# Performance work log

Hardware: AMD Instinct MI355X
Metric: run time of the kernel (lower is better)

## Reference

```python
import jax, jax.numpy as jnp
import numpy as np

VOCAB, EDIM, WFEAT, LABELS, SLOPE = 50000, 128, 128, 2, 0.01
N = 8192

def setup_inputs() -> dict:
    key = jax.random.key(0)
    ks = jax.random.split(key, 8)
    inSen = jax.random.randint(ks[0], (N,), 0, VOCAB, dtype=jnp.int64) if jax.config.read('jax_enable_x64') else jax.random.randint(ks[0], (N,), 0, VOCAB, dtype=jnp.int32)
    adj = jax.random.randint(ks[1], (N, N), 0, 2, dtype=jnp.int32)
    emb = jax.random.normal(ks[2], (VOCAB, EDIM), dtype=jnp.float32)
    W = jax.random.normal(ks[3], (EDIM, WFEAT), dtype=jnp.float32) * (1.0 / np.sqrt(EDIM))
    a_src = jax.random.normal(ks[4], (WFEAT,), dtype=jnp.float32) * (1.0 / np.sqrt(WFEAT))
    a_dst = jax.random.normal(ks[5], (WFEAT,), dtype=jnp.float32) * (1.0 / np.sqrt(WFEAT))
    cls_W = jax.random.normal(ks[6], (WFEAT, LABELS), dtype=jnp.float32) * (1.0 / np.sqrt(WFEAT))
    cls_b = jax.random.normal(ks[7], (LABELS,), dtype=jnp.float32) * 0.01
    return {"inSen": inSen, "adj": adj, "selfLink": 1, "emb": emb, "W": W,
            "a_src": a_src, "a_dst": a_dst, "cls_W": cls_W, "cls_b": cls_b}

def reference(inSen, adj, selfLink, emb, W, a_src, a_dst, cls_W, cls_b):
    # Embedding lookup: (N, edim)
    words = emb[inSen]
    # GAT layer: linear projection then adjacency-masked additive attention
    h = words @ W                              # (N, wFeat)
    f_src = h @ a_src                          # (N,)
    f_dst = h @ a_dst                          # (N,)
    e = jax.nn.leaky_relu(f_src[:, None] + f_dst[None, :], negative_slope=SLOPE)  # (N, N)
    mask = (adj + selfLink * jnp.eye(adj.shape[0], dtype=adj.dtype)) > 0
    e = jnp.where(mask, e, jnp.float32(-1e9))
    attention = jax.nn.softmax(e, axis=1)      # (N, N)
    sentence = attention @ h                   # (N, wFeat)
    # Max pool over words, classify
    poolSentence = jnp.max(sentence, axis=0)   # (wFeat,)
    label = jax.nn.softmax(poolSentence @ cls_W + cls_b, axis=0)  # (labels,)
    return (poolSentence, attention, sentence, label)
```

## Files before the change

kernel.cpp:

```cpp
#include <hip/hip_runtime.h>
#include <hip/hip_bf16.h>

#define NR 8192
#define WF 128

typedef short bf16x8 __attribute__((ext_vector_type(8)));
typedef float f32x4 __attribute__((ext_vector_type(4)));

static __device__ __forceinline__ unsigned int f2bf(float f) {
    unsigned int u = __float_as_uint(f);
    return (u + 0x7fffu + ((u >> 16) & 1u)) >> 16;
}
static __device__ __forceinline__ void atomicMaxF(float* addr, float v) {
    if (v >= 0.f) atomicMax((int*)addr, __float_as_int(v));
    else          atomicMin((unsigned int*)addr, __float_as_uint(v));
}
static __device__ __forceinline__ float lrelu(float x) { return x > 0.f ? x : 0.01f * x; }

__global__ __launch_bounds__(256) void k_proj(
    const int* __restrict__ inSen, const float* __restrict__ emb,
    const float* __restrict__ W, const float* __restrict__ a_src,
    const float* __restrict__ a_dst, float* __restrict__ f_src,
    float* __restrict__ f_dst, float* __restrict__ maxfd,
    unsigned short* __restrict__ hB)
{
    __shared__ float ht[16 * 132];
    const int t = threadIdx.x;
    const int f = t & 127, rh = t >> 7;
    const int i0 = blockIdx.x * 16;

    int wd[8];
    #pragma unroll
    for (int r = 0; r < 8; ++r) wd[r] = inSen[i0 + rh * 8 + r];
    float h[8];
    #pragma unroll
    for (int r = 0; r < 8; ++r) h[r] = 0.f;

    for (int k4 = 0; k4 < 32; ++k4) {
        const float w0 = W[(k4 * 4 + 0) * WF + f];
        const float w1 = W[(k4 * 4 + 1) * WF + f];
        const float w2 = W[(k4 * 4 + 2) * WF + f];
        const float w3 = W[(k4 * 4 + 3) * WF + f];
        #pragma unroll
        for (int r = 0; r < 8; ++r) {
            float4 ev = ((const float4*)(emb + (size_t)wd[r] * 128))[k4];
            h[r] += ev.x * w0 + ev.y * w1 + ev.z * w2 + ev.w * w3;
        }
    }
    #pragma unroll
    for (int r = 0; r < 8; ++r) ht[(rh * 8 + r) * 132 + f] = h[r];
    __syncthreads();

    if (t < 16) {
        float s = 0.f, d = 0.f;
        for (int k4 = 0; k4 < 32; ++k4) {
            float4 hv = *(const float4*)(ht + t * 132 + k4 * 4);
            float4 as = ((const float4*)a_src)[k4];
            float4 ad = ((const float4*)a_dst)[k4];
            s += hv.x * as.x + hv.y * as.y + hv.z * as.z + hv.w * as.w;
            d += hv.x * ad.x + hv.y * ad.y + hv.z * ad.z + hv.w * ad.w;
        }
        f_src[i0 + t] = s;
        f_dst[i0 + t] = d;
        float dm = d;
        #pragma unroll
        for (int o = 1; o < 16; o <<= 1) dm = fmaxf(dm, __shfl_xor(dm, o));
        if (t == 0) atomicMaxF(maxfd, dm);
    }
    {
        const int kb = blockIdx.x >> 1, half = blockIdx.x & 1;
        const int nf = t >> 5, l32 = t & 31;
        const int qloc = l32 >> 4, fx = l32 & 15;
        const int lane = (half * 2 + qloc) * 16 + fx;
        const float* hp = ht + (qloc * 8) * 132 + nf * 16 + fx;
        uint4 v;
        v.x = f2bf(hp[0 * 132]) | (f2bf(hp[1 * 132]) << 16);
        v.y = f2bf(hp[2 * 132]) | (f2bf(hp[3 * 132]) << 16);
        v.z = f2bf(hp[4 * 132]) | (f2bf(hp[5 * 132]) << 16);
        v.w = f2bf(hp[6 * 132]) | (f2bf(hp[7 * 132]) << 16);
        *(uint4*)(hB + ((size_t)kb * 8 + nf) * 512 + lane * 8) = v;
    }
}

static __device__ __forceinline__ void adj_chunk(
    int c, int4 a, float4 f, int lane, int row, int sl,
    float fs, float C, int shl,
    unsigned int* __restrict__ mrow, float& sum)
{
    const bool m0 = a.x > 0, m1 = a.y > 0, m2 = a.z > 0, m3 = a.w > 0;
    float p0 = m0 ? __expf(lrelu(fs + f.x) - C) : 0.f;
    float p1 = m1 ? __expf(lrelu(fs + f.y) - C) : 0.f;
    float p2 = m2 ? __expf(lrelu(fs + f.z) - C) : 0.f;
    float p3 = m3 ? __expf(lrelu(fs + f.w) - C) : 0.f;
    unsigned int nib = (m0 ? 1u : 0u) | (m1 ? 2u : 0u) | (m2 ? 4u : 0u) | (m3 ? 8u : 0u);
    float ssum = p0 + p1 + p2 + p3;
    if (c == (row >> 8)) {
        if (lane == ((row & 255) >> 2)) {
            const int jd = row & 3;
            const int aj = jd == 0 ? a.x : jd == 1 ? a.y : jd == 2 ? a.z : a.w;
            const float fj = jd == 0 ? f.x : jd == 1 ? f.y : jd == 2 ? f.z : f.w;
            const bool mo = aj > 0, mn = (aj + sl) > 0;
            if (mn != mo) {
                const float pd = __expf(lrelu(fs + fj) - C);
                if (mn) { nib |= 1u << jd; ssum += pd; }
                else    { nib &= ~(1u << jd); ssum -= pd; }
            }
        }
    }
    sum += ssum;
    unsigned int v = nib << shl;
    v |= __shfl_xor(v, 1);
    v |= __shfl_xor(v, 2);
    v |= __shfl_xor(v, 4);
    if ((lane & 7) == 0) mrow[c * 8 + (lane >> 3)] = v;
}

__global__ __launch_bounds__(256, 4) void k_adj(
    const int* __restrict__ adj, const int* __restrict__ slP,
    const float* __restrict__ f_src, const float* __restrict__ f_dst,
    const float* __restrict__ maxfd, unsigned int* __restrict__ maskG,
    float* __restrict__ invl)
{
    const int t = threadIdx.x, lane = t & 63, w = t >> 6;
    const int row = blockIdx.x * 4 + w;
    const int sl = slP[0];
    const float fs = f_src[row];
    const float C = lrelu(fs + maxfd[0]);
    const int* __restrict__ ap = adj + (size_t)row * NR + 4 * lane;
    const float* __restrict__ fp = f_dst + 4 * lane;
    unsigned int* __restrict__ mrow = maskG + (size_t)row * 256;
    const int shl = 4 * (lane & 7);
    float sum = 0.f;

    int4   a0 = *(const int4*)(ap + 0 * 256);
    float4 f0 = *(const float4*)(fp + 0 * 256);
    int4   a1 = *(const int4*)(ap + 1 * 256);
    float4 f1 = *(const float4*)(fp + 1 * 256);
    int4   a2 = *(const int4*)(ap + 2 * 256);
    float4 f2 = *(const float4*)(fp + 2 * 256);
    int4   a3 = *(const int4*)(ap + 3 * 256);
    float4 f3 = *(const float4*)(fp + 3 * 256);

    #pragma unroll 1
    for (int c = 0; c < 28; c += 4) {
        int4   n0 = *(const int4*)(ap + (c + 4) * 256);
        float4 g0 = *(const float4*)(fp + (c + 4) * 256);
        int4   n1 = *(const int4*)(ap + (c + 5) * 256);
        float4 g1 = *(const float4*)(fp + (c + 5) * 256);
        int4   n2 = *(const int4*)(ap + (c + 6) * 256);
        float4 g2 = *(const float4*)(fp + (c + 6) * 256);
        int4   n3 = *(const int4*)(ap + (c + 7) * 256);
        float4 g3 = *(const float4*)(fp + (c + 7) * 256);
        adj_chunk(c + 0, a0, f0, lane, row, sl, fs, C, shl, mrow, sum);
        adj_chunk(c + 1, a1, f1, lane, row, sl, fs, C, shl, mrow, sum);
        adj_chunk(c + 2, a2, f2, lane, row, sl, fs, C, shl, mrow, sum);
        adj_chunk(c + 3, a3, f3, lane, row, sl, fs, C, shl, mrow, sum);
        a0 = n0; f0 = g0; a1 = n1; f1 = g1;
        a2 = n2; f2 = g2; a3 = n3; f3 = g3;
    }
    adj_chunk(28, a0, f0, lane, row, sl, fs, C, shl, mrow, sum);
    adj_chunk(29, a1, f1, lane, row, sl, fs, C, shl, mrow, sum);
    adj_chunk(30, a2, f2, lane, row, sl, fs, C, shl, mrow, sum);
    adj_chunk(31, a3, f3, lane, row, sl, fs, C, shl, mrow, sum);

    #pragma unroll
    for (int o = 1; o < 64; o <<= 1) sum += __shfl_xor(sum, o);
    if (lane == 0) invl[row] = 1.0f / sum;
}

__global__ __launch_bounds__(512, 4) void k_att(
    const unsigned int* __restrict__ maskG, const float* __restrict__ f_src,
    const float* __restrict__ f_dst, const float* __restrict__ maxfd,
    const float* __restrict__ invl, const unsigned short* __restrict__ hB,
    float* __restrict__ att, float* __restrict__ sent)
{
    __shared__ float red[8][2048];
    const int t = threadIdx.x;
    const int lane = t & 63, w = t >> 6;
    const int strip = blockIdx.x;
    const int i0 = strip * 16;
    const int fx = lane & 15, quad = lane >> 4;
    const int row = i0 + fx;
    const float fs = f_src[row];
    const float C = lrelu(fs + maxfd[0]);
    const float il = invl[row];
    float* __restrict__ ar = att + (size_t)row * NR;
    const unsigned int* __restrict__ mrow = maskG + (size_t)row * 256;
    f32x4 acc[8] = {};
    const int k0 = w * 1024;

    for (int kk4 = k0; kk4 < k0 + 1024; kk4 += 128) {
        const uint4 mw = *(const uint4*)(mrow + (kk4 >> 5));
        const unsigned int mwa[4] = {mw.x, mw.y, mw.z, mw.w};
        #pragma unroll
        for (int j4 = 0; j4 < 4; ++j4) {
            const int kk = kk4 + j4 * 32;
            const int kb = kk >> 5;
            const unsigned short* hp = hB + (size_t)kb * 4096 + lane * 8;
            bf16x8 bfr[8];
            #pragma unroll
            for (int nf = 0; nf < 8; ++nf) bfr[nf] = *(const bf16x8*)(hp + nf * 512);

            const unsigned int mbyte = (mwa[j4] >> (quad * 8)) & 0xffu;
            const float4 fd0 = *(const float4*)(f_dst + kk + quad * 8);
            const float4 fd1 = *(const float4*)(f_dst + kk + quad * 8 + 4);
            const float fv[8] = {fd0.x, fd0.y, fd0.z, fd0.w, fd1.x, fd1.y, fd1.z, fd1.w};
            float p[8];
            #pragma unroll
            for (int j = 0; j < 8; ++j)
                p[j] = ((mbyte >> j) & 1u) ? __expf(lrelu(fs + fv[j]) - C) : 0.f;

            const float4 w0 = make_float4(p[0] * il, p[1] * il, p[2] * il, p[3] * il);
            const float4 w1 = make_float4(p[4] * il, p[5] * il, p[6] * il, p[7] * il);
            *(float4*)(ar + kk + quad * 8) = w0;
            *(float4*)(ar + kk + quad * 8 + 4) = w1;

            union { uint4 u; bf16x8 v; } cv;
            cv.u.x = f2bf(p[0]) | (f2bf(p[1]) << 16);
            cv.u.y = f2bf(p[2]) | (f2bf(p[3]) << 16);
            cv.u.z = f2bf(p[4]) | (f2bf(p[5]) << 16);
            cv.u.w = f2bf(p[6]) | (f2bf(p[7]) << 16);
            #pragma unroll
            for (int nf = 0; nf < 8; ++nf)
                acc[nf] = __builtin_amdgcn_mfma_f32_16x16x32_bf16(cv.v, bfr[nf], acc[nf], 0, 0, 0);
        }
    }
    #pragma unroll
    for (int reg = 0; reg < 4; ++reg) {
        #pragma unroll
        for (int nf = 0; nf < 8; ++nf)
            red[w][(quad * 4 + reg) * 128 + nf * 16 + fx] = acc[nf][reg];
    }
    __syncthreads();
    {
        const int e0 = t * 4;
        const int m = e0 >> 7, f0 = e0 & 127;
        const float vin = invl[i0 + m];
        float vv[4];
        #pragma unroll
        for (int j = 0; j < 4; ++j) {
            float s = 0.f;
            #pragma unroll
            for (int sx = 0; sx < 8; ++sx) s += red[sx][e0 + j];
            vv[j] = s * vin;
        }
        *(float4*)(sent + (size_t)(i0 + m) * WF + f0) = make_float4(vv[0], vv[1], vv[2], vv[3]);
    }
}

__global__ __launch_bounds__(256) void k_pool(
    const float* __restrict__ sent, float* __restrict__ partial)
{
    __shared__ float s[256];
    const int t = threadIdx.x;
    const int f = t & 127, rh = t >> 7;
    const int r0 = blockIdx.x * 128;
    float m = -1e30f;
    for (int j = 0; j < 64; ++j)
        m = fmaxf(m, sent[(size_t)(r0 + j * 2 + rh) * WF + f]);
    s[t] = m;
    __syncthreads();
    if (t < 128) partial[blockIdx.x * 128 + t] = fmaxf(s[t], s[t + 128]);
}

__global__ __launch_bounds__(128) void k_label(
    const float* __restrict__ partial, const float* __restrict__ cls_W,
    const float* __restrict__ cls_b, float* __restrict__ pool,
    float* __restrict__ label)
{
    __shared__ float s0[128], s1[128];
    const int t = threadIdx.x;
    float m = -1e30f;
    for (int b = 0; b < 64; ++b) m = fmaxf(m, partial[b * 128 + t]);
    pool[t] = m;
    s0[t] = m * cls_W[t * 2 + 0];
    s1[t] = m * cls_W[t * 2 + 1];
    __syncthreads();
    if (t == 0) {
        float z0 = cls_b[0], z1 = cls_b[1];
        for (int f = 0; f < 128; ++f) { z0 += s0[f]; z1 += s1[f]; }
        float mm = fmaxf(z0, z1);
        float e0 = __expf(z0 - mm), e1 = __expf(z1 - mm);
        float inv = 1.0f / (e0 + e1);
        label[0] = e0 * inv;
        label[1] = e1 * inv;
    }
}

extern "C" void kernel_launch(void* const* d_in, const int* in_sizes, int n_in,
                              void* d_out, int out_size, void* d_ws, size_t ws_size,
                              hipStream_t stream)
{
    const int*   inSen    = (const int*)d_in[0];
    const int*   adj      = (const int*)d_in[1];
    const int*   selfLink = (const int*)d_in[2];
    const float* emb      = (const float*)d_in[3];
    const float* W        = (const float*)d_in[4];
    const float* a_src    = (const float*)d_in[5];
    const float* a_dst    = (const float*)d_in[6];
    const float* cls_W    = (const float*)d_in[7];
    const float* cls_b    = (const float*)d_in[8];

    float* out   = (float*)d_out;
    float* pool  = out;
    float* att   = out + 128;
    float* sent  = att + (size_t)NR * NR;
    float* label = sent + (size_t)NR * WF;

    char* ws = (char*)d_ws;
    unsigned short* hB    = (unsigned short*)ws;
    unsigned int*   maskG = (unsigned int*)(ws + (2u << 20));
    float* f_src   = (float*)(ws + (10u << 20));
    float* f_dst   = f_src + NR;
    float* invl    = f_dst + NR;
    float* maxfd   = invl + NR;
    float* partial = maxfd + 64;

    hipMemsetAsync(maxfd, 0xFF, 4, stream);
    k_proj<<<NR / 16, 256, 0, stream>>>(inSen, emb, W, a_src, a_dst, f_src, f_dst, maxfd, hB);
    k_adj<<<NR / 4, 256, 0, stream>>>(adj, selfLink, f_src, f_dst, maxfd, maskG, invl);
    k_att<<<NR / 16, 512, 0, stream>>>(maskG, f_src, f_dst, maxfd, invl, hB, att, sent);
    k_pool<<<NR / 128, 256, 0, stream>>>(sent, partial);
    k_label<<<1, 128, 0, stream>>>(partial, cls_W, cls_b, pool, label);
}
```

Measured before the change: 613.1 us.

## Stage f_dst in LDS and deepen prefetch in adjacency and attention kernels

In the adjacency-mask kernel, each block now copies the whole f_dst vector into shared memory once. The adjacency loads are double-buffered eight chunks deep, where the old code loaded f_dst from global memory in every chunk. The attention kernel is restructured to software-prefetch the next mask words and f_dst values one step ahead of their use. The pooling kernel launches four times as many blocks, each reducing fewer rows, and the label kernel reduces over the larger partial buffer. The aim is more memory-level parallelism on the bandwidth-bound adjacency read, at the cost of 32 KB of LDS per block and more registers, both of which could reduce occupancy.

```diff
diff --git a/kernel.cpp b/kernel.cpp
--- a/kernel.cpp
+++ b/kernel.cpp
@@ -83,10 +83,11 @@
 }
 
 static __device__ __forceinline__ void adj_chunk(
-    int c, int4 a, float4 f, int lane, int row, int sl,
+    int c, int4 a, const float* __restrict__ fdl, int lane, int row, int sl,
     float fs, float C, int shl,
     unsigned int* __restrict__ mrow, float& sum)
 {
+    const float4 f = *(const float4*)(fdl + c * 256 + 4 * lane);
     const bool m0 = a.x > 0, m1 = a.y > 0, m2 = a.z > 0, m3 = a.w > 0;
     float p0 = m0 ? __expf(lrelu(fs + f.x) - C) : 0.f;
     float p1 = m1 ? __expf(lrelu(fs + f.y) - C) : 0.f;
@@ -121,47 +122,47 @@
     const float* __restrict__ maxfd, unsigned int* __restrict__ maskG,
     float* __restrict__ invl)
 {
+    __shared__ float fdl[NR];
     const int t = threadIdx.x, lane = t & 63, w = t >> 6;
     const int row = blockIdx.x * 4 + w;
     const int sl = slP[0];
+    const int* __restrict__ ap = adj + (size_t)row * NR + 4 * lane;
+
+    int4 a0 = *(const int4*)(ap + 0 * 256);
+    int4 a1 = *(const int4*)(ap + 1 * 256);
+    int4 a2 = *(const int4*)(ap + 2 * 256);
+    int4 a3 = *(const int4*)(ap + 3 * 256);
+    int4 a4 = *(const int4*)(ap + 4 * 256);
+    int4 a5 = *(const int4*)(ap + 5 * 256);
+    int4 a6 = *(const int4*)(ap + 6 * 256);
+    int4 a7 = *(const int4*)(ap + 7 * 256);
+
+    #pragma unroll
+    for (int i = 0; i < 8; ++i)
+        *(float4*)(fdl + (i * 256 + t) * 4) = *(const float4*)(f_dst + (i * 256 + t) * 4);
+
     const float fs = f_src[row];
     const float C = lrelu(fs + maxfd[0]);
-    const int* __restrict__ ap = adj + (size_t)row * NR + 4 * lane;
-    const float* __restrict__ fp = f_dst + 4 * lane;
     unsigned int* __restrict__ mrow = maskG + (size_t)row * 256;
     const int shl = 4 * (lane & 7);
     float sum = 0.f;
-
-    int4   a0 = *(const int4*)(ap + 0 * 256);
-    float4 f0 = *(const float4*)(fp + 0 * 256);
-    int4   a1 = *(const int4*)(ap + 1 * 256);
-    float4 f1 = *(const float4*)(fp + 1 * 256);
-    int4   a2 = *(const int4*)(ap + 2 * 256);
-    float4 f2 = *(const float4*)(fp + 2 * 256);
-    int4   a3 = *(const int4*)(ap + 3 * 256);
-    float4 f3 = *(const float4*)(fp + 3 * 256);
-
+    __syncthreads();
+
+    #define ADJC(c, reg) adj_chunk((c), (reg), fdl, lane, row, sl, fs, C, shl, mrow, sum)
     #pragma unroll 1
-    for (int c = 0; c < 28; c += 4) {
-        int4   n0 = *(const int4*)(ap + (c + 4) * 256);
-        float4 g0 = *(const float4*)(fp + (c + 4) * 256);
-        int4   n1 = *(const int4*)(ap + (c + 5) * 256);
-        float4 g1 = *(const float4*)(fp + (c + 5) * 256);
-        int4   n2 = *(const int4*)(ap + (c + 6) * 256);
-        float4 g2 = *(const float4*)(fp + (c + 6) * 256);
-        int4   n3 = *(const int4*)(ap + (c + 7) * 256);
-        float4 g3 = *(const float4*)(fp + (c + 7) * 256);
-        adj_chunk(c + 0, a0, f0, lane, row, sl, fs, C, shl, mrow, sum);
-        adj_chunk(c + 1, a1, f1, lane, row, sl, fs, C, shl, mrow, sum);
-        adj_chunk(c + 2, a2, f2, lane, row, sl, fs, C, shl, mrow, sum);
-        adj_chunk(c + 3, a3, f3, lane, row, sl, fs, C, shl, mrow, sum);
-        a0 = n0; f0 = g0; a1 = n1; f1 = g1;
-        a2 = n2; f2 = g2; a3 = n3; f3 = g3;
-    }
-    adj_chunk(28, a0, f0, lane, row, sl, fs, C, shl, mrow, sum);
-    adj_chunk(29, a1, f1, lane, row, sl, fs, C, shl, mrow, sum);
-    adj_chunk(30, a2, f2, lane, row, sl, fs, C, shl, mrow, sum);
-    adj_chunk(31, a3, f3, lane, row, sl, fs, C, shl, mrow, sum);
+    for (int g = 0; g < 24; g += 8) {
+        ADJC(g + 0, a0); a0 = *(const int4*)(ap + (g +  8) * 256);
+        ADJC(g + 1, a1); a1 = *(const int4*)(ap + (g +  9) * 256);
+        ADJC(g + 2, a2); a2 = *(const int4*)(ap + (g + 10) * 256);
+        ADJC(g + 3, a3); a3 = *(const int4*)(ap + (g + 11) * 256);
+        ADJC(g + 4, a4); a4 = *(const int4*)(ap + (g + 12) * 256);
+        ADJC(g + 5, a5); a5 = *(const int4*)(ap + (g + 13) * 256);
+        ADJC(g + 6, a6); a6 = *(const int4*)(ap + (g + 14) * 256);
+        ADJC(g + 7, a7); a7 = *(const int4*)(ap + (g + 15) * 256);
+    }
+    ADJC(24, a0); ADJC(25, a1); ADJC(26, a2); ADJC(27, a3);
+    ADJC(28, a4); ADJC(29, a5); ADJC(30, a6); ADJC(31, a7);
+    #undef ADJC
 
     #pragma unroll
     for (int o = 1; o < 64; o <<= 1) sum += __shfl_xor(sum, o);
@@ -187,29 +188,42 @@
     float* __restrict__ ar = att + (size_t)row * NR;
     const unsigned int* __restrict__ mrow = maskG + (size_t)row * 256;
     f32x4 acc[8] = {};
-    const int k0 = w * 1024;
-
-    for (int kk4 = k0; kk4 < k0 + 1024; kk4 += 128) {
-        const uint4 mw = *(const uint4*)(mrow + (kk4 >> 5));
-        const unsigned int mwa[4] = {mw.x, mw.y, mw.z, mw.w};
-        #pragma unroll
-        for (int j4 = 0; j4 < 4; ++j4) {
-            const int kk = kk4 + j4 * 32;
-            const int kb = kk >> 5;
-            const unsigned short* hp = hB + (size_t)kb * 4096 + lane * 8;
+    const int kb0 = w * 32;
+    const unsigned short* __restrict__ hp0 = hB + (size_t)kb0 * 4096 + lane * 8;
+    const float* __restrict__ fp0 = f_dst + kb0 * 32 + quad * 8;
+
+    uint4 mw = *(const uint4*)(mrow + kb0);
+    float4 fdA0 = *(const float4*)(fp0);
+    float4 fdA1 = *(const float4*)(fp0 + 4);
+
+    #pragma unroll 1
+    for (int g = 0; g < 8; ++g) {
+        uint4 mw_n;
+        if (g < 7) mw_n = *(const uint4*)(mrow + kb0 + (g + 1) * 4);
+        #pragma unroll
+        for (int j = 0; j < 4; ++j) {
+            const int i = g * 4 + j;
+            const unsigned short* hp = hp0 + (size_t)i * 4096;
             bf16x8 bfr[8];
             #pragma unroll
             for (int nf = 0; nf < 8; ++nf) bfr[nf] = *(const bf16x8*)(hp + nf * 512);
-
-            const unsigned int mbyte = (mwa[j4] >> (quad * 8)) & 0xffu;
-            const float4 fd0 = *(const float4*)(f_dst + kk + quad * 8);
-            const float4 fd1 = *(const float4*)(f_dst + kk + quad * 8 + 4);
-            const float fv[8] = {fd0.x, fd0.y, fd0.z, fd0.w, fd1.x, fd1.y, fd1.z, fd1.w};
+            float4 fdB0, fdB1;
+            {
+                const float* fpn = fp0 + (i + 1) * 32;
+                fdB0 = *(const float4*)(fpn);
+                fdB1 = *(const float4*)(fpn + 4);
+            }
+            const unsigned int mword = (j == 0) ? mw.x : (j == 1) ? mw.y
+                                     : (j == 2) ? mw.z : mw.w;
+            const unsigned int mbyte = (mword >> (quad * 8)) & 0xffu;
+            const float fv[8] = {fdA0.x, fdA0.y, fdA0.z, fdA0.w,
+                                 fdA1.x, fdA1.y, fdA1.z, fdA1.w};
             float p[8];
             #pragma unroll
-            for (int j = 0; j < 8; ++j)
-                p[j] = ((mbyte >> j) & 1u) ? __expf(lrelu(fs + fv[j]) - C) : 0.f;
-
+            for (int jj = 0; jj < 8; ++jj)
+                p[jj] = ((mbyte >> jj) & 1u) ? __expf(lrelu(fs + fv[jj]) - C) : 0.f;
+
+            const int kk = (kb0 + i) * 32;
             const float4 w0 = make_float4(p[0] * il, p[1] * il, p[2] * il, p[3] * il);
             const float4 w1 = make_float4(p[4] * il, p[5] * il, p[6] * il, p[7] * il);
             *(float4*)(ar + kk + quad * 8) = w0;
@@ -223,7 +237,9 @@
             #pragma unroll
             for (int nf = 0; nf < 8; ++nf)
                 acc[nf] = __builtin_amdgcn_mfma_f32_16x16x32_bf16(cv.v, bfr[nf], acc[nf], 0, 0, 0);
-        }
+            fdA0 = fdB0; fdA1 = fdB1;
+        }
+        if (g < 7) mw = mw_n;
     }
     #pragma unroll
     for (int reg = 0; reg < 4; ++reg) {
@@ -254,9 +270,10 @@
     __shared__ float s[256];
     const int t = threadIdx.x;
     const int f = t & 127, rh = t >> 7;
-    const int r0 = blockIdx.x * 128;
+    const int r0 = blockIdx.x * 32;
     float m = -1e30f;
-    for (int j = 0; j < 64; ++j)
+    #pragma unroll
+    for (int j = 0; j < 16; ++j)
         m = fmaxf(m, sent[(size_t)(r0 + j * 2 + rh) * WF + f]);
     s[t] = m;
     __syncthreads();
@@ -271,7 +288,7 @@
     __shared__ float s0[128], s1[128];
     const int t = threadIdx.x;
     float m = -1e30f;
-    for (int b = 0; b < 64; ++b) m = fmaxf(m, partial[b * 128 + t]);
+    for (int b = 0; b < 256; ++b) m = fmaxf(m, partial[b * 128 + t]);
     pool[t] = m;
     s0[t] = m * cls_W[t * 2 + 0];
     s1[t] = m * cls_W[t * 2 + 1];
@@ -320,6 +337,6 @@
     k_proj<<<NR / 16, 256, 0, stream>>>(inSen, emb, W, a_src, a_dst, f_src, f_dst, maxfd, hB);
     k_adj<<<NR / 4, 256, 0, stream>>>(adj, selfLink, f_src, f_dst, maxfd, maskG, invl);
     k_att<<<NR / 16, 512, 0, stream>>>(maskG, f_src, f_dst, maxfd, invl, hB, att, sent);
-    k_pool<<<NR / 128, 256, 0, stream>>>(sent, partial);
+    k_pool<<<NR / 32, 256, 0, stream>>>(sent, partial);
     k_label<<<1, 128, 0, stream>>>(partial, cls_W, cls_b, pool, label);
 }
```

Measured after the change: 626.0 us. +2.1%, slower.
